# Performance work log

Measured on AMD Instinct MI355X. Metric: run time of the kernel, lower is better.

Reference implementation:

```python
import jax, jax.numpy as jnp
import numpy as np

N_NODES = 10000
E = 160000
MUL_NB = 16      # irreps_sh_neighbor = 16x0e + 16x1o
MUL_S = 32       # scalars in edge_fea (32x0e)
MUL_V = 16       # vectors in edge_fea (16x1o)
S1M = 2 * MUL_NB # 32 scalars in concatenated edge_sh_neighbor
V1M = 2 * MUL_NB # 32 vectors in concatenated edge_sh_neighbor
OUT_S = 48       # 32 activated scalars + 16 gate scalars (0e)
OUT_V = 16       # 16x1o gated vectors


def setup_inputs() -> dict:
    key = jax.random.key(0)
    k = jax.random.split(key, 16)

    def p(i, shape, scale=1.0):
        return scale * jax.random.normal(k[i], shape, jnp.float32)

    return dict(
        edge_sh=p(0, (E, 4)),
        edge_fea=p(1, (E, MUL_S + 3 * MUL_V)),
        edge_index=jax.random.randint(k[2], (2, E), 0, N_NODES),
        batch_edge=jnp.zeros((E,), jnp.int32),
        w1=p(3, (MUL_S, 64), 1.0 / np.sqrt(MUL_S)), b1=jnp.zeros((64,), jnp.float32),
        w2=p(4, (64, 64), 0.125), b2=jnp.zeros((64,), jnp.float32),
        w3=p(5, (64, 4 * MUL_NB), 0.125), b3=jnp.zeros((4 * MUL_NB,), jnp.float32),
        w_ss=p(6, (OUT_S, S1M, MUL_S)),
        w_vv=p(7, (OUT_S, V1M, MUL_V)),
        w_sv=p(8, (OUT_V, S1M, MUL_V)),
        w_vs=p(9, (OUT_V, V1M, MUL_S)),
    )


def reference(edge_sh, edge_fea, edge_index, batch_edge, w1, b1, w2, b2, w3, b3,
              w_ss, w_vv, w_sv, w_vs):
    silu = jax.nn.silu
    # Extract tr=+1 scalars and run the per-edge weight MLP (scalar_len -> 64 -> 64 -> 2*weight_numel)
    s_fea = edge_fea[:, :MUL_S]
    h = silu(s_fea @ w1 + b1)
    h = silu(h @ w2 + b2)
    weight = h @ w3 + b3                                   # [E, 2*weight_numel]

    def mix(w):
        # e3nn Linear (1x0e+1x1o -> 16x0e+16x1o) with external per-edge weights
        ws, wv = w[:, :MUL_NB], w[:, MUL_NB:]
        s = ws * edge_sh[:, :1]                            # [E,16]
        v = wv[:, :, None] * edge_sh[:, None, 1:4]         # [E,16,3]
        return s, v

    half = weight.shape[-1] // 2
    si, vi = mix(weight[:, :half])
    sj, vj = mix(weight[:, half:])
    idx_i, idx_j = edge_index[0], edge_index[1]
    seg = lambda x: jax.ops.segment_sum(x, idx_i, num_segments=N_NODES)
    # NOTE: the original scatters BOTH halves with index_i, then gathers with index_i / index_j
    S1 = jnp.concatenate([seg(si)[idx_i], seg(sj)[idx_j]], axis=-1)  # [E,32]
    V1 = jnp.concatenate([seg(vi)[idx_i], seg(vj)[idx_j]], axis=1)   # [E,32,3]

    S2 = edge_fea[:, :MUL_S]
    V2 = edge_fea[:, MUL_S:].reshape(E, MUL_V, 3)

    c3 = 1.0 / np.sqrt(3.0)    # CG coefficient for 1o x 1o -> 0e
    inv2 = 1.0 / np.sqrt(2.0)  # path-count normalization (2 paths per output irrep)
    o_s = inv2 * (
        jnp.einsum('ei,ej,oij->eo', S1, S2, w_ss) / np.sqrt(S1M * MUL_S)
        + c3 * jnp.einsum('eic,ejc,oij->eo', V1, V2, w_vv) / np.sqrt(V1M * MUL_V)
    )                                                       # [E,48]
    o_v = inv2 * (
        jnp.einsum('ei,ejc,oij->eoc', S1, V2, w_sv) / np.sqrt(S1M * MUL_V)
        + jnp.einsum('eic,ej,oij->eoc', V1, S2, w_vs) / np.sqrt(V1M * MUL_S)
    )                                                       # [E,16,3]
    # Gate nonlinearity: silu on scalars, sigmoid gates on vectors
    s_out = silu(o_s[:, :MUL_S])
    gates = jax.nn.sigmoid(o_s[:, MUL_S:])
    v_out = o_v * gates[:, :, None]
    return jnp.concatenate([s_out, v_out.reshape(E, 3 * OUT_V)], axis=-1)
```

## Files before the change

### kernel.cpp

```cpp
#include <hip/hip_runtime.h>
#include <hip/hip_bf16.h>

#define EDGES 160000
#define NNODES 10000

typedef __attribute__((ext_vector_type(8))) short short8;
typedef __attribute__((ext_vector_type(4))) float f32x4;

__device__ __forceinline__ float fsigmoid(float x) {
    return 1.0f / (1.0f + __expf(-x));
}

union F8 { uint32_t u[4]; short8 s8; };

__device__ __forceinline__ uint32_t pk2(float e0, float e1) {
    uint32_t r;
    asm("v_cvt_pk_bf16_f32 %0, %1, %2" : "=v"(r) : "v"(e0), "v"(e1));
    return r;
}

__device__ __forceinline__ void split8(const float* x, F8& ah, F8& al) {
    #pragma unroll
    for (int r = 0; r < 4; ++r) {
        const float x0 = x[2*r], x1 = x[2*r+1];
        const uint32_t h = pk2(x0, x1);
        ah.u[r] = h;
        const float f0 = __uint_as_float(h << 16);
        const float f1 = __uint_as_float(h & 0xffff0000u);
        al.u[r] = pk2(x0 - f0, x1 - f1);
    }
}

__device__ __forceinline__ f32x4 mm(const F8& a, const F8& b, f32x4 c) {
    return __builtin_amdgcn_mfma_f32_16x16x32_bf16(a.s8, b.s8, c, 0, 0, 0);
}

__device__ __forceinline__ void ld_b(const uint4* p, int idx, F8& d) {
    const uint4 v = p[idx];
    d.u[0] = v.x; d.u[1] = v.y; d.u[2] = v.z; d.u[3] = v.w;
}

extern "C" __global__ void __launch_bounds__(256)
k_hist(const int* __restrict__ idx_i, int* __restrict__ counts)
{
    const int e = blockIdx.x * 256 + threadIdx.x;
    if (e < EDGES) atomicAdd(&counts[idx_i[e]], 1);
}

extern "C" __global__ void __launch_bounds__(256)
k_scan(const int* __restrict__ counts, int* __restrict__ offsets,
       int* __restrict__ cursor)
{
    __shared__ int sc[2][256];
    const int t = threadIdx.x;
    const int base = t * 40;
    int loc[40];
    int s = 0;
    #pragma unroll
    for (int k = 0; k < 40; ++k) {
        const int idx = base + k;
        const int c = (idx < NNODES) ? counts[idx] : 0;
        loc[k] = c; s += c;
    }
    sc[0][t] = s;
    __syncthreads();
    int src = 0;
    for (int off = 1; off < 256; off <<= 1) {
        int v = sc[src][t];
        if (t >= off) v += sc[src][t - off];
        sc[src ^ 1][t] = v;
        __syncthreads();
        src ^= 1;
    }
    int run = sc[src][t] - s;
    #pragma unroll
    for (int k = 0; k < 40; ++k) {
        const int idx = base + k;
        if (idx < NNODES) {
            offsets[idx] = run;
            cursor[idx]  = run;
            run += loc[k];
        }
    }
    if (t == 255) offsets[NNODES] = EDGES;
}

extern "C" __global__ void __launch_bounds__(256)
k_pack_mlp(const float* __restrict__ w1, const float* __restrict__ w2,
           const float* __restrict__ w3, uint4* __restrict__ pkw)
{
    const int t = blockIdx.x * 256 + threadIdx.x;
    const float* W; int local;
    if (t < 512)       { W = w1; local = t; }
    else if (t < 1536) { W = w2; local = t - 512; }
    else               { W = w3; local = t - 1536; }

    const int l    = local & 63;
    const int h    = (local >> 6) & 1;
    const int rest = local >> 7;
    const int nt   = rest & 3;
    const int kc   = rest >> 2;
    const int n    = nt*16 + (l & 15);
    const int kb   = kc*32 + (l >> 4)*8;

    uint32_t out[4];
    #pragma unroll
    for (int r = 0; r < 4; ++r) {
        const float x0 = W[(size_t)(kb + 2*r    )*64 + n];
        const float x1 = W[(size_t)(kb + 2*r + 1)*64 + n];
        const uint32_t hi = pk2(x0, x1);
        if (h == 0) out[r] = hi;
        else {
            const float f0 = __uint_as_float(hi << 16);
            const float f1 = __uint_as_float(hi & 0xffff0000u);
            out[r] = pk2(x0 - f0, x1 - f1);
        }
    }
    pkw[t] = make_uint4(out[0], out[1], out[2], out[3]);
}

extern "C" __global__ void __launch_bounds__(256, 2)
k_mlp_mfma(const float* __restrict__ edge_sh,
           const float* __restrict__ edge_fea,
           const int* __restrict__ idx_i,
           const float* __restrict__ b1, const float* __restrict__ b2,
           const float* __restrict__ b3,
           const uint4* __restrict__ pkw,
           int* __restrict__ cursor,
           float* __restrict__ wgtbuf, float* __restrict__ shbuf)
{
    __shared__ float sAbuf[4][64*68];
    __shared__ int   sSlot[256];

    const int tid = threadIdx.x;
    const int w   = tid >> 6, l = tid & 63;
    const int r16 = l & 15, ks = l >> 4;
    const int e0w = blockIdx.x * 256 + w * 64;
    float* A = sAbuf[w];

    {
        const int eg = e0w + l;
        const int ni = idx_i[eg];
        const int slot = atomicAdd(&cursor[ni], 1);
        sSlot[tid] = slot;
        *reinterpret_cast<float4*>(shbuf + (size_t)slot * 4) =
            *reinterpret_cast<const float4*>(edge_sh + (size_t)eg * 4);
    }

    f32x4 acc[4][4];

    {
        float bias[4];
        #pragma unroll
        for (int nt = 0; nt < 4; ++nt) bias[nt] = b1[nt*16 + r16];
        #pragma unroll
        for (int mt = 0; mt < 4; ++mt)
            #pragma unroll
            for (int nt = 0; nt < 4; ++nt)
                acc[mt][nt] = (f32x4){bias[nt], bias[nt], bias[nt], bias[nt]};

        F8 ah[4], al[4];
        #pragma unroll
        for (int mt = 0; mt < 4; ++mt) {
            const float* src = edge_fea + (size_t)(e0w + mt*16 + r16)*80 + ks*8;
            const float4 v0 = *reinterpret_cast<const float4*>(src);
            const float4 v1 = *reinterpret_cast<const float4*>(src + 4);
            float x[8];
            x[0]=v0.x; x[1]=v0.y; x[2]=v0.z; x[3]=v0.w;
            x[4]=v1.x; x[5]=v1.y; x[6]=v1.z; x[7]=v1.w;
            split8(x, ah[mt], al[mt]);
        }
        #pragma unroll
        for (int nt = 0; nt < 4; ++nt) {
            F8 bh, bl;
            ld_b(pkw, (nt*2 + 0)*64 + l, bh);
            ld_b(pkw, (nt*2 + 1)*64 + l, bl);
            #pragma unroll
            for (int mt = 0; mt < 4; ++mt) {
                acc[mt][nt] = mm(ah[mt], bh, acc[mt][nt]);
                acc[mt][nt] = mm(al[mt], bh, acc[mt][nt]);
                acc[mt][nt] = mm(ah[mt], bl, acc[mt][nt]);
            }
        }
        #pragma unroll
        for (int mt = 0; mt < 4; ++mt)
            #pragma unroll
            for (int nt = 0; nt < 4; ++nt)
                #pragma unroll
                for (int r = 0; r < 4; ++r) {
                    const float v = acc[mt][nt][r];
                    A[(mt*16 + ks*4 + r)*68 + nt*16 + r16] = v * fsigmoid(v);
                }
    }

    #pragma unroll 1
    for (int layer = 0; layer < 2; ++layer) {
        const uint4* pkl = pkw + 512 + layer*1024;
        const float* bb  = (layer == 0) ? b2 : b3;
        float bias[4];
        #pragma unroll
        for (int nt = 0; nt < 4; ++nt) bias[nt] = bb[nt*16 + r16];
        #pragma unroll
        for (int mt = 0; mt < 4; ++mt)
            #pragma unroll
            for (int nt = 0; nt < 4; ++nt)
                acc[mt][nt] = (f32x4){bias[nt], bias[nt], bias[nt], bias[nt]};

        #pragma unroll
        for (int kc = 0; kc < 2; ++kc) {
            F8 ah[4], al[4];
            #pragma unroll
            for (int mt = 0; mt < 4; ++mt) {
                const float* src = A + (mt*16 + r16)*68 + kc*32 + ks*8;
                const float4 v0 = *reinterpret_cast<const float4*>(src);
                const float4 v1 = *reinterpret_cast<const float4*>(src + 4);
                float x[8];
                x[0]=v0.x; x[1]=v0.y; x[2]=v0.z; x[3]=v0.w;
                x[4]=v1.x; x[5]=v1.y; x[6]=v1.z; x[7]=v1.w;
                split8(x, ah[mt], al[mt]);
            }
            #pragma unroll
            for (int nt = 0; nt < 4; ++nt) {
                F8 bh, bl;
                ld_b(pkl, ((kc*4 + nt)*2 + 0)*64 + l, bh);
                ld_b(pkl, ((kc*4 + nt)*2 + 1)*64 + l, bl);
                #pragma unroll
                for (int mt = 0; mt < 4; ++mt) {
                    acc[mt][nt] = mm(ah[mt], bh, acc[mt][nt]);
                    acc[mt][nt] = mm(al[mt], bh, acc[mt][nt]);
                    acc[mt][nt] = mm(ah[mt], bl, acc[mt][nt]);
                }
            }
        }
        if (layer == 0) {
            #pragma unroll
            for (int mt = 0; mt < 4; ++mt)
                #pragma unroll
                for (int nt = 0; nt < 4; ++nt)
                    #pragma unroll
                    for (int r = 0; r < 4; ++r) {
                        const float v = acc[mt][nt][r];
                        A[(mt*16 + ks*4 + r)*68 + nt*16 + r16] = v * fsigmoid(v);
                    }
        }
    }

    #pragma unroll
    for (int mt = 0; mt < 4; ++mt) {
        int sl[4];
        #pragma unroll
        for (int r = 0; r < 4; ++r)
            sl[r] = sSlot[(tid & ~63) + mt*16 + ks*4 + r];
        #pragma unroll
        for (int nt = 0; nt < 4; ++nt)
            #pragma unroll
            for (int r = 0; r < 4; ++r)
                wgtbuf[(size_t)sl[r]*64 + nt*16 + r16] = acc[mt][nt][r];
    }
}

extern "C" __global__ void __launch_bounds__(256)
k_reduce(const int* __restrict__ offsets,
         const float* __restrict__ wgtbuf, const float* __restrict__ shbuf,
         float* __restrict__ nsI, float* __restrict__ nsJ,
         float* __restrict__ nvI, float* __restrict__ nvJ)
{
    const int tid = threadIdx.x;
    const int n = blockIdx.x * 2 + (tid >> 7);
    const int o = tid & 127;

    int widx, shc;
    float* dst;
    if (o < 16)      { widx = o;            shc = 0;     dst = &nsI[n*16 + o]; }
    else if (o < 64) { const int r = o - 16; const int m = r / 3, c = r - 3*m;
                       widx = 16 + m;       shc = 1 + c; dst = &nvI[(n*16 + m)*3 + c]; }
    else if (o < 80) { const int r = o - 64;
                       widx = 32 + r;       shc = 0;     dst = &nsJ[n*16 + r]; }
    else             { const int r = o - 80; const int m = r / 3, c = r - 3*m;
                       widx = 48 + m;       shc = 1 + c; dst = &nvJ[(n*16 + m)*3 + c]; }

    const int s0 = offsets[n], s1 = offsets[n + 1];
    float acc = 0.0f;
    for (int s = s0; s < s1; ++s)
        acc = fmaf(wgtbuf[(size_t)s*64 + widx], shbuf[(size_t)s*4 + shc], acc);
    *dst = acc;
}

extern "C" __global__ void __launch_bounds__(256)
k_pack(const float* __restrict__ w_ss, const float* __restrict__ w_vv,
       const float* __restrict__ w_sv, const float* __restrict__ w_vs,
       uint4* __restrict__ pk)
{
    const int t = blockIdx.x * 256 + threadIdx.x;
    const float INV2  = 0.70710678118654752f;
    const float RS512 = 22.627416997969522f;
    const float C3    = 0.57735026918962576f;

    const float* W; int K; float scale; int local; int tiles;
    if (t < 12288)      { W = w_ss; K = 1024; scale = INV2/32.0f;     local = t;         tiles = 3; }
    else if (t < 18432) { W = w_vv; K = 512;  scale = INV2*C3/RS512;  local = t - 12288; tiles = 3; }
    else if (t < 20480) { W = w_sv; K = 512;  scale = INV2/RS512;     local = t - 18432; tiles = 1; }
    else                { W = w_vs; K = 1024; scale = INV2/32.0f;     local = t - 20480; tiles = 1; }

    const int l    = local & 63;
    const int h    = (local >> 6) & 1;
    const int rest = local >> 7;
    const int tile = rest % tiles;
    const int kc   = rest / tiles;
    const int o    = tile*16 + (l & 15);
    const int kb   = kc*32 + (l >> 4)*8;

    const float4* src = reinterpret_cast<const float4*>(W + (size_t)o * K + kb);
    const float4 a = src[0], b = src[1];
    const float v[8] = {a.x, a.y, a.z, a.w, b.x, b.y, b.z, b.w};

    uint32_t out[4];
    #pragma unroll
    for (int r = 0; r < 4; ++r) {
        const float x0 = v[2*r] * scale, x1 = v[2*r+1] * scale;
        const uint32_t hi = pk2(x0, x1);
        if (h == 0) out[r] = hi;
        else {
            const float f0 = __uint_as_float(hi << 16);
            const float f1 = __uint_as_float(hi & 0xffff0000u);
            out[r] = pk2(x0 - f0, x1 - f1);
        }
    }
    pk[t] = make_uint4(out[0], out[1], out[2], out[3]);
}

extern "C" __global__ void __launch_bounds__(512)
k_contract(const float* __restrict__ edge_fea,
           const int* __restrict__ idx_i, const int* __restrict__ idx_j,
           const float* __restrict__ nsI, const float* __restrict__ nsJ,
           const float* __restrict__ nvI, const float* __restrict__ nvJ,
           const uint4* __restrict__ pk,
           float* __restrict__ out)
{
    __shared__ float lds[13568];
    float* sS1T = lds;
    float* sS2  = lds + 2048;
    float* sV1T = lds + 4160;
    float* sV2  = lds + 10304;
    float* sOs  = lds;
    float* sOv  = lds + 4160;

    const int tid = threadIdx.x;
    const int e0  = blockIdx.x * 64;

    for (int t = tid; t < 64*20; t += 512) {
        const int ge = t & 63, qd = t >> 6;
        const float4 v = *reinterpret_cast<const float4*>(
            edge_fea + (size_t)(e0 + ge) * 80 + qd * 4);
        const float vv4[4] = {v.x, v.y, v.z, v.w};
        #pragma unroll
        for (int u = 0; u < 4; ++u) {
            const int f = qd*4 + u;
            if (f < 32) sS2[ge*33 + f] = vv4[u];
            else {
                const int r = f - 32;
                sV2[(r % 3)*1088 + ge*17 + r/3] = vv4[u];
            }
        }
    }
    for (int t = tid; t < 2048; t += 512) {
        const int ge = t & 63, i = t >> 6;
        const float v = (i < 16) ? nsI[idx_i[e0+ge]*16 + i]
                                 : nsJ[idx_j[e0+ge]*16 + (i - 16)];
        sS1T[i*64 + ge] = v;
    }
    for (int t = tid; t < 6144; t += 512) {
        const int ge = t & 63, r = t >> 6;
        const int i = r / 3, c = r % 3;
        const float v = (i < 16) ? nvI[(idx_i[e0+ge]*16 + i)*3 + c]
                                 : nvJ[(idx_j[e0+ge]*16 + (i - 16))*3 + c];
        sV1T[c*2048 + i*64 + ge] = v;
    }
    __syncthreads();

    const int w  = tid >> 6;
    const int l  = tid & 63;
    const int q  = w & 3;
    const int e  = q*16 + (l & 15);
    const int ks = l >> 4;

    const uint4* Bss = pk;
    const uint4* Bvv = pk + 12288;
    const uint4* Bsv = pk + 18432;
    const uint4* Bvs = pk + 20480;

    float s2r[8];
    #pragma unroll
    for (int u = 0; u < 8; ++u) s2r[u] = sS2[e*33 + ks*8 + u];
    float v2r[3][8];
    #pragma unroll
    for (int c = 0; c < 3; ++c)
        #pragma unroll
        for (int u = 0; u < 8; ++u)
            v2r[c][u] = sV2[c*1088 + e*17 + (ks & 1)*8 + u];

    f32x4 acc[3] = {{0,0,0,0},{0,0,0,0},{0,0,0,0}};

    if (w < 4) {
        for (int i = 0; i < 32; ++i) {
            const float s1 = sS1T[i*64 + e];
            float x[8];
            #pragma unroll
            for (int u = 0; u < 8; ++u) x[u] = s1 * s2r[u];
            F8 ah, al; split8(x, ah, al);
            #pragma unroll
            for (int t = 0; t < 3; ++t) {
                F8 bh, bl;
                ld_b(Bss, ((i*3 + t)*2 + 0)*64 + l, bh);
                ld_b(Bss, ((i*3 + t)*2 + 1)*64 + l, bl);
                acc[t] = mm(ah, bh, acc[t]);
                acc[t] = mm(al, bh, acc[t]);
                acc[t] = mm(ah, bl, acc[t]);
            }
        }
        for (int n = 0; n < 16; ++n) {
            const int i = 2*n + (ks >> 1);
            const float a0 = sV1T[0*2048 + i*64 + e];
            const float a1 = sV1T[1*2048 + i*64 + e];
            const float a2 = sV1T[2*2048 + i*64 + e];
            float x[8];
            #pragma unroll
            for (int u = 0; u < 8; ++u)
                x[u] = fmaf(a2, v2r[2][u], fmaf(a1, v2r[1][u], a0 * v2r[0][u]));
            F8 ah, al; split8(x, ah, al);
            #pragma unroll
            for (int t = 0; t < 3; ++t) {
                F8 bh, bl;
                ld_b(Bvv, ((n*3 + t)*2 + 0)*64 + l, bh);
                ld_b(Bvv, ((n*3 + t)*2 + 1)*64 + l, bl);
                acc[t] = mm(ah, bh, acc[t]);
                acc[t] = mm(al, bh, acc[t]);
                acc[t] = mm(ah, bl, acc[t]);
            }
        }
    } else {
        for (int n = 0; n < 16; ++n) {
            const int i = 2*n + (ks >> 1);
            const float s1 = sS1T[i*64 + e];
            F8 bh, bl;
            ld_b(Bsv, (n*2 + 0)*64 + l, bh);
            ld_b(Bsv, (n*2 + 1)*64 + l, bl);
            #pragma unroll
            for (int c = 0; c < 3; ++c) {
                float x[8];
                #pragma unroll
                for (int u = 0; u < 8; ++u) x[u] = s1 * v2r[c][u];
                F8 ah, al; split8(x, ah, al);
                acc[c] = mm(ah, bh, acc[c]);
                acc[c] = mm(al, bh, acc[c]);
                acc[c] = mm(ah, bl, acc[c]);
            }
        }
        for (int i = 0; i < 32; ++i) {
            F8 bh, bl;
            ld_b(Bvs, (i*2 + 0)*64 + l, bh);
            ld_b(Bvs, (i*2 + 1)*64 + l, bl);
            #pragma unroll
            for (int c = 0; c < 3; ++c) {
                const float v1 = sV1T[c*2048 + i*64 + e];
                float x[8];
                #pragma unroll
                for (int u = 0; u < 8; ++u) x[u] = v1 * s2r[u];
                F8 ah, al; split8(x, ah, al);
                acc[c] = mm(ah, bh, acc[c]);
                acc[c] = mm(al, bh, acc[c]);
                acc[c] = mm(ah, bl, acc[c]);
            }
        }
    }

    __syncthreads();

    if (w < 4) {
        #pragma unroll
        for (int t = 0; t < 3; ++t)
            #pragma unroll
            for (int r = 0; r < 4; ++r)
                sOs[(t*16 + (l & 15))*65 + q*16 + ks*4 + r] = acc[t][r];
    } else {
        #pragma unroll
        for (int c = 0; c < 3; ++c)
            #pragma unroll
            for (int r = 0; r < 4; ++r)
                sOv[((l & 15)*3 + c)*65 + q*16 + ks*4 + r] = acc[c][r];
    }
    __syncthreads();

    for (int t = tid; t < 64*80; t += 512) {
        const int ge = t / 80, f = t % 80;
        float r;
        if (f < 32) {
            const float xv = sOs[f*65 + ge];
            r = xv * fsigmoid(xv);
        } else {
            const int rr = f - 32;
            const int o  = rr / 3;
            r = sOv[rr*65 + ge] * fsigmoid(sOs[(32 + o)*65 + ge]);
        }
        out[(size_t)(e0 + ge)*80 + f] = r;
    }
}

extern "C" void kernel_launch(void* const* d_in, const int* in_sizes, int n_in,
                              void* d_out, int out_size, void* d_ws, size_t ws_size,
                              hipStream_t stream)
{
    const float* edge_sh  = (const float*)d_in[0];
    const float* edge_fea = (const float*)d_in[1];
    const int*   eidx     = (const int*)d_in[2];
    const float* w1 = (const float*)d_in[4];
    const float* b1 = (const float*)d_in[5];
    const float* w2 = (const float*)d_in[6];
    const float* b2 = (const float*)d_in[7];
    const float* w3 = (const float*)d_in[8];
    const float* b3 = (const float*)d_in[9];
    const float* w_ss = (const float*)d_in[10];
    const float* w_vv = (const float*)d_in[11];
    const float* w_sv = (const float*)d_in[12];
    const float* w_vs = (const float*)d_in[13];
    float* out = (float*)d_out;

    float* ws  = (float*)d_ws;
    float* nsI = ws;
    float* nsJ = ws + 160000;
    float* nvI = ws + 320000;
    float* nvJ = ws + 800000;
    float* wgtbuf = ws + 1280000;
    float* shbuf  = ws + 11520000;
    int*   counts  = (int*)(ws + 12160000);
    int*   offsets = counts + NNODES;
    int*   cursor  = offsets + NNODES + 1;
    uint4* pkbuf = (uint4*)wgtbuf;
    uint4* pkw = (uint4*)d_out;

    hipMemsetAsync(counts, 0, NNODES * sizeof(int), stream);
    k_hist<<<625, 256, 0, stream>>>(eidx, counts);
    k_scan<<<1, 256, 0, stream>>>(counts, offsets, cursor);
    k_pack_mlp<<<10, 256, 0, stream>>>(w1, w2, w3, pkw);
    k_mlp_mfma<<<625, 256, 0, stream>>>(edge_sh, edge_fea, eidx,
                                        b1, b2, b3, pkw,
                                        cursor, wgtbuf, shbuf);
    k_reduce<<<NNODES/2, 256, 0, stream>>>(offsets, wgtbuf, shbuf,
                                           nsI, nsJ, nvI, nvJ);
    k_pack<<<96, 256, 0, stream>>>(w_ss, w_vv, w_sv, w_vs, pkbuf);
    k_contract<<<2500, 512, 0, stream>>>(edge_fea, eidx, eidx + EDGES,
                                         nsI, nsJ, nvI, nvJ, pkbuf, out);
}
```

Measured before the change: 416.5 us.

## Factor vector-output paths into MFMA contraction then per-edge FMA with transposed V2

For the w_sv and w_vs paths, the kernel now contracts the shared scalar operand with the weights once via MFMA, producing per-(edge, output, j) partials. It then multiplies these by the three vector components with scalar FMAs, instead of running three separate MFMA chains over outer-product inputs. The weight packing for w_sv and w_vs is reordered to match the new K ordering. V2 is stored transposed in LDS so it can be read as float4 per edge group. This removes about two thirds of the MFMA and split work in half of the waves. In exchange it holds large register arrays (m3 with 16 entries, m4 with 32 f32x4), which may raise register pressure or cause spills.

Result: slower. 450.7 us (+8.2%).

```diff
diff --git a/kernel.cpp b/kernel.cpp
--- a/kernel.cpp
+++ b/kernel.cpp
@@ -296,28 +296,47 @@
     const float RS512 = 22.627416997969522f;
     const float C3    = 0.57735026918962576f;
 
-    const float* W; int K; float scale; int local; int tiles;
-    if (t < 12288)      { W = w_ss; K = 1024; scale = INV2/32.0f;     local = t;         tiles = 3; }
-    else if (t < 18432) { W = w_vv; K = 512;  scale = INV2*C3/RS512;  local = t - 12288; tiles = 3; }
-    else if (t < 20480) { W = w_sv; K = 512;  scale = INV2/RS512;     local = t - 18432; tiles = 1; }
-    else                { W = w_vs; K = 1024; scale = INV2/32.0f;     local = t - 20480; tiles = 1; }
-
-    const int l    = local & 63;
-    const int h    = (local >> 6) & 1;
-    const int rest = local >> 7;
-    const int tile = rest % tiles;
-    const int kc   = rest / tiles;
-    const int o    = tile*16 + (l & 15);
-    const int kb   = kc*32 + (l >> 4)*8;
-
-    const float4* src = reinterpret_cast<const float4*>(W + (size_t)o * K + kb);
-    const float4 a = src[0], b = src[1];
-    const float v[8] = {a.x, a.y, a.z, a.w, b.x, b.y, b.z, b.w};
+    float v8[8];
+    float scale;
+
+    if (t < 18432) {
+        const float* W; int K; int local; int tiles;
+        if (t < 12288) { W = w_ss; K = 1024; scale = INV2/32.0f;    local = t;         tiles = 3; }
+        else           { W = w_vv; K = 512;  scale = INV2*C3/RS512; local = t - 12288; tiles = 3; }
+        const int l    = local & 63;
+        const int rest = local >> 7;
+        const int tile = rest % tiles;
+        const int kc   = rest / tiles;
+        const int o    = tile*16 + (l & 15);
+        const int kb   = kc*32 + (l >> 4)*8;
+        #pragma unroll
+        for (int u = 0; u < 8; ++u) v8[u] = W[(size_t)o * K + kb + u];
+    } else if (t < 20480) {
+        const int local = t - 18432;
+        const int l = local & 63;
+        const int j = local >> 7;
+        const int o = l & 15;
+        const int kb = (l >> 4)*8;
+        scale = INV2 / RS512;
+        #pragma unroll
+        for (int u = 0; u < 8; ++u) v8[u] = w_sv[o*512 + (kb + u)*16 + j];
+    } else {
+        const int local = t - 20480;
+        const int l = local & 63;
+        const int i = local >> 7;
+        const int o = l & 15;
+        const int kb = (l >> 4)*8;
+        scale = INV2 / 32.0f;
+        #pragma unroll
+        for (int u = 0; u < 8; ++u) v8[u] = w_vs[o*1024 + i*32 + kb + u];
+    }
+
+    const int h = (((t < 18432) ? t : (t < 20480 ? t - 18432 : t - 20480)) >> 6) & 1;
 
     uint32_t out[4];
     #pragma unroll
     for (int r = 0; r < 4; ++r) {
-        const float x0 = v[2*r] * scale, x1 = v[2*r+1] * scale;
+        const float x0 = v8[2*r] * scale, x1 = v8[2*r+1] * scale;
         const uint32_t hi = pk2(x0, x1);
         if (h == 0) out[r] = hi;
         else {
@@ -337,11 +356,11 @@
            const uint4* __restrict__ pk,
            float* __restrict__ out)
 {
-    __shared__ float lds[13568];
+    __shared__ float lds[13376];
     float* sS1T = lds;
     float* sS2  = lds + 2048;
     float* sV1T = lds + 4160;
-    float* sV2  = lds + 10304;
+    float* sV2T = lds + 10304;
     float* sOs  = lds;
     float* sOv  = lds + 4160;
 
@@ -359,7 +378,7 @@
             if (f < 32) sS2[ge*33 + f] = vv4[u];
             else {
                 const int r = f - 32;
-                sV2[(r % 3)*1088 + ge*17 + r/3] = vv4[u];
+                sV2T[(r % 3)*1024 + (r/3)*64 + ge] = vv4[u];
             }
         }
     }
@@ -392,16 +411,17 @@
     float s2r[8];
     #pragma unroll
     for (int u = 0; u < 8; ++u) s2r[u] = sS2[e*33 + ks*8 + u];
-    float v2r[3][8];
-    #pragma unroll
-    for (int c = 0; c < 3; ++c)
-        #pragma unroll
-        for (int u = 0; u < 8; ++u)
-            v2r[c][u] = sV2[c*1088 + e*17 + (ks & 1)*8 + u];
 
     f32x4 acc[3] = {{0,0,0,0},{0,0,0,0},{0,0,0,0}};
 
     if (w < 4) {
+        float v2r[3][8];
+        #pragma unroll
+        for (int c = 0; c < 3; ++c)
+            #pragma unroll
+            for (int u = 0; u < 8; ++u)
+                v2r[c][u] = sV2T[c*1024 + ((ks & 1)*8 + u)*64 + e];
+
         for (int i = 0; i < 32; ++i) {
             const float s1 = sS1T[i*64 + e];
             float x[8];
@@ -439,37 +459,65 @@
             }
         }
     } else {
-        for (int n = 0; n < 16; ++n) {
-            const int i = 2*n + (ks >> 1);
-            const float s1 = sS1T[i*64 + e];
-            F8 bh, bl;
-            ld_b(Bsv, (n*2 + 0)*64 + l, bh);
-            ld_b(Bsv, (n*2 + 1)*64 + l, bl);
-            #pragma unroll
-            for (int c = 0; c < 3; ++c) {
-                float x[8];
+        const int er = q*16 + ks*4;
+
+        {
+            float s1r[8];
+            #pragma unroll
+            for (int u = 0; u < 8; ++u) s1r[u] = sS1T[(ks*8 + u)*64 + e];
+            F8 a1h, a1l; split8(s1r, a1h, a1l);
+
+            f32x4 m3[16];
+            #pragma unroll
+            for (int j = 0; j < 16; ++j) {
+                F8 bh, bl;
+                ld_b(Bsv, (j*2 + 0)*64 + l, bh);
+                ld_b(Bsv, (j*2 + 1)*64 + l, bl);
+                f32x4 d = {0,0,0,0};
+                d = mm(a1h, bh, d);
+                d = mm(a1l, bh, d);
+                d = mm(a1h, bl, d);
+                m3[j] = d;
+            }
+            #pragma unroll
+            for (int j = 0; j < 16; ++j) {
                 #pragma unroll
-                for (int u = 0; u < 8; ++u) x[u] = s1 * v2r[c][u];
-                F8 ah, al; split8(x, ah, al);
-                acc[c] = mm(ah, bh, acc[c]);
-                acc[c] = mm(al, bh, acc[c]);
-                acc[c] = mm(ah, bl, acc[c]);
-            }
-        }
-        for (int i = 0; i < 32; ++i) {
-            F8 bh, bl;
-            ld_b(Bvs, (i*2 + 0)*64 + l, bh);
-            ld_b(Bvs, (i*2 + 1)*64 + l, bl);
-            #pragma unroll
-            for (int c = 0; c < 3; ++c) {
-                const float v1 = sV1T[c*2048 + i*64 + e];
-                float x[8];
+                for (int c = 0; c < 3; ++c) {
+                    const float4 v2 = *reinterpret_cast<const float4*>(
+                        &sV2T[c*1024 + j*64 + er]);
+                    acc[c][0] = fmaf(v2.x, m3[j][0], acc[c][0]);
+                    acc[c][1] = fmaf(v2.y, m3[j][1], acc[c][1]);
+                    acc[c][2] = fmaf(v2.z, m3[j][2], acc[c][2]);
+                    acc[c][3] = fmaf(v2.w, m3[j][3], acc[c][3]);
+                }
+            }
+        }
+        {
+            F8 a2h, a2l; split8(s2r, a2h, a2l);
+
+            f32x4 m4[32];
+            #pragma unroll
+            for (int i = 0; i < 32; ++i) {
+                F8 bh, bl;
+                ld_b(Bvs, (i*2 + 0)*64 + l, bh);
+                ld_b(Bvs, (i*2 + 1)*64 + l, bl);
+                f32x4 d = {0,0,0,0};
+                d = mm(a2h, bh, d);
+                d = mm(a2l, bh, d);
+                d = mm(a2h, bl, d);
+                m4[i] = d;
+            }
+            #pragma unroll
+            for (int i = 0; i < 32; ++i) {
                 #pragma unroll
-                for (int u = 0; u < 8; ++u) x[u] = v1 * s2r[u];
-                F8 ah, al; split8(x, ah, al);
-                acc[c] = mm(ah, bh, acc[c]);
-                acc[c] = mm(al, bh, acc[c]);
-                acc[c] = mm(ah, bl, acc[c]);
+                for (int c = 0; c < 3; ++c) {
+                    const float4 v1 = *reinterpret_cast<const float4*>(
+                        &sV1T[c*2048 + i*64 + er]);
+                    acc[c][0] = fmaf(v1.x, m4[i][0], acc[c][0]);
+                    acc[c][1] = fmaf(v1.y, m4[i][1], acc[c][1]);
+                    acc[c][2] = fmaf(v1.z, m4[i][2], acc[c][2]);
+                    acc[c][3] = fmaf(v1.w, m4[i][3], acc[c][3]);
+                }
             }
         }
     }
```
